# Kernel optimization log

Measured on AMD Instinct MI355X. Metric: run time of the kernel, lower is better.

The kernel has to match this reference:

```python
import jax, jax.numpy as jnp
import numpy as np

B, T, D, H, O = 64, 512, 512, 512, 1

def setup_inputs() -> dict:
    key = jax.random.key(0)
    ks = jax.random.split(key, 12)
    s_in = 1.0 / np.sqrt(H)
    inp = {
        'x': jax.random.normal(ks[0], (B, T, D), dtype=jnp.float32),
        'W_ih0': jax.random.uniform(ks[1], (H, D), jnp.float32, -s_in, s_in),
        'W_hh0': jax.random.uniform(ks[2], (H, H), jnp.float32, -s_in, s_in),
        'b_ih0': jax.random.uniform(ks[3], (H,), jnp.float32, -s_in, s_in),
        'b_hh0': jax.random.uniform(ks[4], (H,), jnp.float32, -s_in, s_in),
        'W_ih1': jax.random.uniform(ks[5], (H, H), jnp.float32, -s_in, s_in),
        'W_hh1': jax.random.uniform(ks[6], (H, H), jnp.float32, -s_in, s_in),
        'b_ih1': jax.random.uniform(ks[7], (H,), jnp.float32, -s_in, s_in),
        'b_hh1': jax.random.uniform(ks[8], (H,), jnp.float32, -s_in, s_in),
        'W_fc': jax.random.uniform(ks[9], (O, H), jnp.float32, -s_in, s_in),
        'b_fc': jax.random.uniform(ks[10], (O,), jnp.float32, -s_in, s_in),
    }
    return inp

def _rnn_layer(inp, W_ih, W_hh, b_ih, b_hh):
    # inp: [B, T, Din] -> [B, T, H].  h_t = tanh(x_t W_ih^T + b_ih + h_{t-1} W_hh^T + b_hh)
    xproj = jnp.einsum('btd,hd->bth', inp, W_ih) + b_ih + b_hh  # precompute input projection
    h0 = jnp.zeros((inp.shape[0], W_hh.shape[0]), inp.dtype)
    def step(h, xp):  # xp: [B, H]
        h = jnp.tanh(xp + h @ W_hh.T)
        return h, h
    _, outs = jax.lax.scan(step, h0, jnp.swapaxes(xproj, 0, 1))  # [T, B, H]
    return jnp.swapaxes(outs, 0, 1)

def reference(x, W_ih0, W_hh0, b_ih0, b_hh0, W_ih1, W_hh1, b_ih1, b_hh1, W_fc, b_fc):
    h = _rnn_layer(x, W_ih0, W_hh0, b_ih0, b_hh0)
    h = _rnn_layer(h, W_ih1, W_hh1, b_ih1, b_hh1)
    last = h[:, -1, :]                      # [B, H]
    return last @ W_fc.T + b_fc             # [B, O]
```

## Files before the change

kernel.cpp:

```cpp
#include <hip/hip_runtime.h>
#include <cstdint>
#include <cstddef>

typedef _Float16 f16;
typedef _Float16 half2_t __attribute__((ext_vector_type(2)));
typedef _Float16 half4_t __attribute__((ext_vector_type(4)));
typedef _Float16 half8_t __attribute__((ext_vector_type(8)));
typedef float floatx4 __attribute__((ext_vector_type(4)));

__device__ __forceinline__ float fdot2u(uint32_t w, uint32_t h, float acc) {
#if __has_builtin(__builtin_amdgcn_fdot2)
    return __builtin_amdgcn_fdot2(__builtin_bit_cast(half2_t, w),
                                  __builtin_bit_cast(half2_t, h), acc, false);
#else
    half2_t a = __builtin_bit_cast(half2_t, w);
    half2_t b = __builtin_bit_cast(half2_t, h);
    return acc + (float)a[0] * (float)b[0] + (float)a[1] * (float)b[1];
#endif
}

__device__ __forceinline__ void spin_ge(int* f, int v) {
    while (__hip_atomic_load(f, __ATOMIC_RELAXED, __HIP_MEMORY_SCOPE_AGENT) < v)
        __builtin_amdgcn_s_sleep(16);
}

__device__ __forceinline__ void acq_fence() {
    __builtin_amdgcn_fence(__ATOMIC_ACQUIRE, "agent");
}

__global__ void cvt_kernel(const float* __restrict__ in, f16* __restrict__ out, int n4) {
    int i = blockIdx.x * blockDim.x + threadIdx.x;
    int stride = gridDim.x * blockDim.x;
    const float4* in4 = (const float4*)in;
    for (; i < n4; i += stride) {
        float4 v = in4[i];
        half4_t h = {(f16)v.x, (f16)v.y, (f16)v.z, (f16)v.w};
        *(half4_t*)&out[(size_t)i * 4] = h;
    }
}

__global__ void bsum_kernel(const float* __restrict__ a, const float* __restrict__ b,
                            float* __restrict__ o) {
    int i = threadIdx.x;
    o[i] = a[i] + b[i];
}

__global__ void pack_whh(const float* __restrict__ W, uint32_t* __restrict__ wp) {
    int id = blockIdx.x * 256 + threadIdx.x;
    int j = id >> 8;
    int kp = id & 255;
    int k = kp * 2;
    int w = j >> 6, jsub = (j >> 3) & 7, r = j & 7;
    int kg = k >> 6, c = (k >> 3) & 7, q = (k >> 1) & 3;
    int tid = w * 64 + jsub * 8 + kg;
    int idx = c * 32 + r * 4 + q;
    uint32_t lo = (uint32_t)__builtin_bit_cast(uint16_t, (f16)W[(size_t)j * 512 + k]);
    uint32_t hi = (uint32_t)__builtin_bit_cast(uint16_t, (f16)W[(size_t)j * 512 + k + 1]);
    size_t off;
    if (idx < 224) off = (size_t)idx * 512 + tid;
    else           off = (size_t)224 * 512 + ((size_t)(r * 512 + tid)) * 4 + q;
    wp[off] = (hi << 16) | lo;
}

__global__ __launch_bounds__(256) void gemm_xp(const f16* __restrict__ A,
                                               const f16* __restrict__ Bw,
                                               const float* __restrict__ bias,
                                               f16* __restrict__ C) {
    const int bn = blockIdx.x & 3;
    const int bm = blockIdx.x >> 2;
    const int tid = threadIdx.x;
    const int w = tid >> 6, l = tid & 63;
    const int wr = w >> 1, wc = w & 1;
    __shared__ f16 As[128 * 32];
    __shared__ f16 Bs[128 * 32];
    floatx4 acc[4][4] = {};
    const int lr = l & 15, lk = (l >> 4) * 8;
    for (int kk = 0; kk < 512; kk += 32) {
        __syncthreads();
        uint4 av[2], bv[2];
#pragma unroll
        for (int s = 0; s < 2; ++s) {
            int chunk = tid + s * 256;
            int row = chunk >> 2;
            int colh = (chunk & 3) * 8;
            av[s] = *(const uint4*)&A[((size_t)(bm * 128 + row)) * 512 + kk + colh];
            bv[s] = *(const uint4*)&Bw[((size_t)(bn * 128 + row)) * 512 + kk + colh];
        }
#pragma unroll
        for (int s = 0; s < 2; ++s) {
            int chunk = tid + s * 256;
            *(uint4*)&As[chunk * 8] = av[s];
            *(uint4*)&Bs[chunk * 8] = bv[s];
        }
        __syncthreads();
        half8_t af[4], bf[4];
#pragma unroll
        for (int m = 0; m < 4; ++m)
            af[m] = *(const half8_t*)&As[(wr * 64 + m * 16 + lr) * 32 + lk];
#pragma unroll
        for (int n = 0; n < 4; ++n)
            bf[n] = *(const half8_t*)&Bs[(wc * 64 + n * 16 + lr) * 32 + lk];
#pragma unroll
        for (int m = 0; m < 4; ++m)
#pragma unroll
            for (int n = 0; n < 4; ++n)
                acc[m][n] = __builtin_amdgcn_mfma_f32_16x16x32_f16(af[m], bf[n], acc[m][n], 0, 0, 0);
    }
    float bz[4];
#pragma unroll
    for (int n = 0; n < 4; ++n) bz[n] = bias[bn * 128 + wc * 64 + n * 16 + lr];
    const int lq = l >> 4;
#pragma unroll
    for (int m = 0; m < 4; ++m)
#pragma unroll
        for (int n = 0; n < 4; ++n)
#pragma unroll
            for (int e = 0; e < 4; ++e) {
                int row = bm * 128 + wr * 64 + m * 16 + lq * 4 + e;
                int col = bn * 128 + wc * 64 + n * 16 + lr;
                C[(size_t)row * 512 + col] = (f16)(acc[m][n][e] + bz[n]);
            }
}

#define FOR_Q(M, c, r) M(c, r, 0) M(c, r, 1) M(c, r, 2) M(c, r, 3)
#define FOR_R8(M, c) FOR_Q(M, c, 0) FOR_Q(M, c, 1) FOR_Q(M, c, 2) FOR_Q(M, c, 3) \
                     FOR_Q(M, c, 4) FOR_Q(M, c, 5) FOR_Q(M, c, 6) FOR_Q(M, c, 7)
#define FOR_ALL(M) FOR_R8(M, 0) FOR_R8(M, 1) FOR_R8(M, 2) FOR_R8(M, 3) \
                   FOR_R8(M, 4) FOR_R8(M, 5) FOR_R8(M, 6)

#define DECLW(c, r, q) uint32_t W_##c##_##r##_##q;
#define LOADW(c, r, q) W_##c##_##r##_##q = wpb[(size_t)(((c)*32 + (r)*4 + (q)) * 512) + tid];
#define DOTQ(c, r, q) a##r = fdot2u(W_##c##_##r##_##q, hq##q, a##r);

#define CHUNK(c)                                                   \
    {                                                              \
        uint4 hv = *(const uint4*)(hrow + (c) * 4);                \
        uint32_t hq0 = hv.x, hq1 = hv.y, hq2 = hv.z, hq3 = hv.w;   \
        FOR_R8(DOTQ, c)                                            \
    }

#define LROW(r)                                                    \
    {                                                              \
        uint4 wv = *(const uint4*)&wlds[((r) * 512 + tid) * 4];    \
        a##r = fdot2u(wv.x, hq0, a##r);                            \
        a##r = fdot2u(wv.y, hq1, a##r);                            \
        a##r = fdot2u(wv.z, hq2, a##r);                            \
        a##r = fdot2u(wv.w, hq3, a##r);                            \
    }

#define CHUNKL                                                     \
    {                                                              \
        uint4 hv = *(const uint4*)(hrow + 7 * 4);                  \
        uint32_t hq0 = hv.x, hq1 = hv.y, hq2 = hv.z, hq3 = hv.w;   \
        LROW(0) LROW(1) LROW(2) LROW(3)                            \
        LROW(4) LROW(5) LROW(6) LROW(7)                            \
    }

#define TREE8                                                                 \
    float b0 = (m0 ? a1 : a0) + __shfl_xor(m0 ? a0 : a1, 1);                  \
    float b1 = (m0 ? a3 : a2) + __shfl_xor(m0 ? a2 : a3, 1);                  \
    float b2 = (m0 ? a5 : a4) + __shfl_xor(m0 ? a4 : a5, 1);                  \
    float b3 = (m0 ? a7 : a6) + __shfl_xor(m0 ? a6 : a7, 1);                  \
    float c0 = (m1 ? b1 : b0) + __shfl_xor(m1 ? b0 : b1, 2);                  \
    float c1 = (m1 ? b3 : b2) + __shfl_xor(m1 ? b2 : b3, 2);                  \
    float d0 = (m2 ? c1 : c0) + __shfl_xor(m2 ? c0 : c1, 4);

#define HB_STRIDE 72
#define XROW 576

__global__ __launch_bounds__(512)
__attribute__((amdgpu_waves_per_eu(2, 2)))
void fused3(const f16* __restrict__ xp0, const uint32_t* __restrict__ wp0,
            const uint32_t* __restrict__ wpih1, const uint32_t* __restrict__ wp1,
            const float* __restrict__ bs1,
            f16* __restrict__ h0seq, f16* __restrict__ xp1seq,
            f16* __restrict__ h1last,
            int* __restrict__ flag1, int* __restrict__ flag2) {
    const int xcd = blockIdx.x & 7;
    if (xcd >= 6) return;
    const int stage = xcd >> 1;
    const int row = (xcd & 1) * 32 + (blockIdx.x >> 3);
    const int tid = threadIdx.x;
    const int kg = tid & 7;
    __shared__ alignas(16) f16 hbuf[2][8 * HB_STRIDE];
    __shared__ uint32_t wlds[8 * 512 * 4];
    __shared__ alignas(16) f16 xin[2][16 * XROW];

    const uint32_t* wpb = (stage == 0) ? wp0 : (stage == 1) ? wpih1 : wp1;
    const f16* inbase = (stage == 0) ? xp0 + (size_t)row * 262144
                       : (stage == 1) ? h0seq + (size_t)row * 262144
                                      : xp1seq + (size_t)row * 262144;
    f16* outbase = (stage == 0) ? h0seq + (size_t)row * 262144
                  : (stage == 1) ? xp1seq + (size_t)row * 262144
                                 : h1last + (size_t)row * 512;
    int* flIn  = (stage == 1) ? flag1 + row : (stage == 2) ? flag2 + row : nullptr;
    int* flOut = (stage == 0) ? flag1 + row : (stage == 1) ? flag2 + row : nullptr;

    auto stageChunk = [&](int g) {
#pragma unroll
        for (int s2 = 0; s2 < 2; ++s2) {
            int s = tid + s2 * 512;
            int rw = s >> 6, pos = s & 63;
            uint4 v = *(const uint4*)&inbase[(size_t)(g * 16 + rw) * 512 + pos * 8];
            *(uint4*)&xin[g & 1][rw * XROW + (pos >> 3) * 72 + (pos & 7) * 8] = v;
        }
    };

    FOR_ALL(DECLW)
    FOR_ALL(LOADW)
#pragma unroll
    for (int i = 0; i < 8; ++i) {
        uint4 v = *(const uint4*)&wpb[(size_t)224 * 512 + (size_t)(i * 512 + tid) * 4];
        *(uint4*)&wlds[(i * 512 + tid) * 4] = v;
    }
    for (int i = tid; i < 2 * 8 * HB_STRIDE; i += 512) ((f16*)hbuf)[i] = (f16)0.f;
    float bsv = (stage == 1) ? bs1[tid] : 0.f;

    if (flIn) {
        spin_ge(flIn, 1);
        acq_fence();
    }
    stageChunk(0);
    __syncthreads();

    const bool m0 = (tid & 1), m1 = (tid & 2), m2 = (tid & 4);
    const int hwpos = (tid >> 6) * HB_STRIDE + (tid & 63);

    if (stage == 1) {
        for (int c = 0; c < 32; ++c) {
            for (int lt = 0; lt < 16; ++lt) {
                if (lt == 12 && c < 31) {
                    spin_ge(flIn, c + 2);
                    acq_fence();
                    stageChunk(c + 1);
                }
                float a0 = 0.f, a1 = 0.f, a2 = 0.f, a3 = 0.f;
                float a4 = 0.f, a5 = 0.f, a6 = 0.f, a7 = 0.f;
                const uint32_t* hrow = (const uint32_t*)&xin[c & 1][lt * XROW + kg * 72];
                CHUNKL
                CHUNK(0) CHUNK(1) CHUNK(2) CHUNK(3) CHUNK(4) CHUNK(5) CHUNK(6)
                TREE8
                outbase[(size_t)(c * 16 + lt) * 512 + tid] = (f16)(d0 + bsv);
            }
            __syncthreads();
            if (tid == 0)
                __hip_atomic_store(flOut, c + 1, __ATOMIC_RELEASE, __HIP_MEMORY_SCOPE_AGENT);
        }
    } else {
        int p = 0;
        for (int t = 0; t < 512; ++t) {
            const int c = t >> 4, lt = t & 15;
            if (lt == 12 && c < 31) {
                if (flIn) {
                    spin_ge(flIn, c + 2);
                    acq_fence();
                }
                stageChunk(c + 1);
            }
            float xpv = (float)xin[c & 1][lt * XROW + (tid >> 6) * 72 + (tid & 63)];

            float a0 = 0.f, a1 = 0.f, a2 = 0.f, a3 = 0.f;
            float a4 = 0.f, a5 = 0.f, a6 = 0.f, a7 = 0.f;
            const uint32_t* hrow = (const uint32_t*)&hbuf[p][kg * HB_STRIDE];
            CHUNKL
            CHUNK(0) CHUNK(1) CHUNK(2) CHUNK(3) CHUNK(4) CHUNK(5) CHUNK(6)
            TREE8
            float s = d0 + xpv;
            float e = __expf(2.0f * s);
            f16 hh = (f16)(1.0f - 2.0f / (1.0f + e));
            hbuf[p ^ 1][hwpos] = hh;
            if (stage == 0) outbase[(size_t)t * 512 + tid] = hh;
            else if (t == 511) outbase[tid] = hh;
            __syncthreads();
            if (stage == 0 && lt == 15 && tid == 0)
                __hip_atomic_store(flOut, c + 1, __ATOMIC_RELEASE, __HIP_MEMORY_SCOPE_AGENT);
            p ^= 1;
        }
    }
}

__global__ __launch_bounds__(512) void fc_kernel(const f16* __restrict__ h1,
                                                 const float* __restrict__ Wfc,
                                                 const float* __restrict__ bfc,
                                                 float* __restrict__ out) {
    int b = blockIdx.x, tid = threadIdx.x;
    __shared__ float red[8];
    float v = (float)h1[(size_t)b * 512 + tid] * Wfc[tid];
#pragma unroll
    for (int off = 32; off > 0; off >>= 1) v += __shfl_down(v, off, 64);
    if ((tid & 63) == 0) red[tid >> 6] = v;
    __syncthreads();
    if (tid == 0) {
        float s = bfc[0];
#pragma unroll
        for (int g = 0; g < 8; ++g) s += red[g];
        out[b] = s;
    }
}

extern "C" void kernel_launch(void* const* d_in, const int* in_sizes, int n_in,
                              void* d_out, int out_size, void* d_ws, size_t ws_size,
                              hipStream_t stream) {
    const float* x    = (const float*)d_in[0];
    const float* Wih0 = (const float*)d_in[1];
    const float* Whh0 = (const float*)d_in[2];
    const float* bih0 = (const float*)d_in[3];
    const float* bhh0 = (const float*)d_in[4];
    const float* Wih1 = (const float*)d_in[5];
    const float* Whh1 = (const float*)d_in[6];
    const float* bih1 = (const float*)d_in[7];
    const float* bhh1 = (const float*)d_in[8];
    const float* Wfc  = (const float*)d_in[9];
    const float* bfc  = (const float*)d_in[10];
    float* out = (float*)d_out;

    char* ws = (char*)d_ws;
    size_t off = 0;
    auto alloc = [&](size_t bytes) -> void* {
        void* p = ws + off;
        off += (bytes + 255) & ~(size_t)255;
        return p;
    };
    const size_t MTD = (size_t)64 * 512 * 512;
    f16* x16    = (f16*)alloc(MTD * 2);
    f16* h016   = (f16*)alloc(MTD * 2);
    f16* xpb    = (f16*)alloc(MTD * 2);
    f16* xp1b   = (f16*)alloc(MTD * 2);
    f16* wih016 = (f16*)alloc((size_t)512 * 512 * 2);
    uint32_t* wp0   = (uint32_t*)alloc((size_t)131072 * 4);
    uint32_t* wp1   = (uint32_t*)alloc((size_t)131072 * 4);
    uint32_t* wpih1 = (uint32_t*)alloc((size_t)131072 * 4);
    float* bs0 = (float*)alloc(512 * 4);
    float* bs1 = (float*)alloc(512 * 4);
    f16* h1last = (f16*)alloc((size_t)64 * 512 * 2);
    int* flags = (int*)alloc(128 * 4);

    cvt_kernel<<<2048, 256, 0, stream>>>(x, x16, (int)(MTD / 4));
    cvt_kernel<<<256, 256, 0, stream>>>(Wih0, wih016, 512 * 512 / 4);
    bsum_kernel<<<1, 512, 0, stream>>>(bih0, bhh0, bs0);
    bsum_kernel<<<1, 512, 0, stream>>>(bih1, bhh1, bs1);
    pack_whh<<<512, 256, 0, stream>>>(Whh0, wp0);
    pack_whh<<<512, 256, 0, stream>>>(Whh1, wp1);
    pack_whh<<<512, 256, 0, stream>>>(Wih1, wpih1);
    (void)hipMemsetAsync(flags, 0, 128 * 4, stream);

    gemm_xp<<<1024, 256, 0, stream>>>(x16, wih016, bs0, xpb);
    fused3<<<256, 512, 0, stream>>>(xpb, wp0, wpih1, wp1, bs1,
                                    h016, xp1b, h1last, flags, flags + 64);
    fc_kernel<<<64, 512, 0, stream>>>(h1last, Wfc, bfc, out);
}
```

Baseline: 1.172 ms.

## Halve inter-stage chunk size and prefetch up to three chunks ahead

Measured after the change: 1.489 ms. 27.1% more time.

```diff
diff --git a/kernel.cpp b/kernel.cpp
--- a/kernel.cpp
+++ b/kernel.cpp
@@ -184,7 +184,8 @@
     const int kg = tid & 7;
     __shared__ alignas(16) f16 hbuf[2][8 * HB_STRIDE];
     __shared__ uint32_t wlds[8 * 512 * 4];
-    __shared__ alignas(16) f16 xin[2][16 * XROW];
+    __shared__ alignas(16) f16 xin[4][8 * XROW];
+    __shared__ int availLds;
 
     const uint32_t* wpb = (stage == 0) ? wp0 : (stage == 1) ? wpih1 : wp1;
     const f16* inbase = (stage == 0) ? xp0 + (size_t)row * 262144
@@ -197,13 +198,9 @@
     int* flOut = (stage == 0) ? flag1 + row : (stage == 1) ? flag2 + row : nullptr;
 
     auto stageChunk = [&](int g) {
-#pragma unroll
-        for (int s2 = 0; s2 < 2; ++s2) {
-            int s = tid + s2 * 512;
-            int rw = s >> 6, pos = s & 63;
-            uint4 v = *(const uint4*)&inbase[(size_t)(g * 16 + rw) * 512 + pos * 8];
-            *(uint4*)&xin[g & 1][rw * XROW + (pos >> 3) * 72 + (pos & 7) * 8] = v;
-        }
+        int rw = tid >> 6, pos = tid & 63;
+        uint4 v = *(const uint4*)&inbase[(size_t)(g * 8 + rw) * 512 + pos * 8];
+        *(uint4*)&xin[g & 3][rw * XROW + (pos >> 3) * 72 + (pos & 7) * 8] = v;
     };
 
     FOR_ALL(DECLW)
@@ -227,37 +224,65 @@
     const int hwpos = (tid >> 6) * HB_STRIDE + (tid & 63);
 
     if (stage == 1) {
-        for (int c = 0; c < 32; ++c) {
-            for (int lt = 0; lt < 16; ++lt) {
-                if (lt == 12 && c < 31) {
-                    spin_ge(flIn, c + 2);
-                    acq_fence();
-                    stageChunk(c + 1);
+        int fetched = 0, availB = 1;
+        for (int c = 0; c < 64; ++c) {
+            for (int lt = 0; lt < 8; ++lt) {
+                if (lt == 4) {
+                    if (fetched < c + 1 && c < 63) {
+                        spin_ge(flIn, c + 2);
+                        acq_fence();
+                        stageChunk(c + 1);
+                        fetched = c + 1;
+                    }
+                    int lim = (c + 3 < 63) ? c + 3 : 63;
+                    int target = (availB - 1 < lim) ? availB - 1 : lim;
+                    if (target > fetched) {
+                        acq_fence();
+                        for (int g = fetched + 1; g <= target; ++g) stageChunk(g);
+                        fetched = target;
+                    }
                 }
                 float a0 = 0.f, a1 = 0.f, a2 = 0.f, a3 = 0.f;
                 float a4 = 0.f, a5 = 0.f, a6 = 0.f, a7 = 0.f;
-                const uint32_t* hrow = (const uint32_t*)&xin[c & 1][lt * XROW + kg * 72];
+                const uint32_t* hrow = (const uint32_t*)&xin[c & 3][lt * XROW + kg * 72];
                 CHUNKL
                 CHUNK(0) CHUNK(1) CHUNK(2) CHUNK(3) CHUNK(4) CHUNK(5) CHUNK(6)
                 TREE8
-                outbase[(size_t)(c * 16 + lt) * 512 + tid] = (f16)(d0 + bsv);
+                outbase[(size_t)(c * 8 + lt) * 512 + tid] = (f16)(d0 + bsv);
             }
+            if (tid == 0)
+                availLds = __hip_atomic_load(flIn, __ATOMIC_RELAXED, __HIP_MEMORY_SCOPE_AGENT);
             __syncthreads();
+            availB = availLds;
             if (tid == 0)
                 __hip_atomic_store(flOut, c + 1, __ATOMIC_RELEASE, __HIP_MEMORY_SCOPE_AGENT);
         }
     } else {
-        int p = 0;
+        int p = 0, fetched = 0;
         for (int t = 0; t < 512; ++t) {
-            const int c = t >> 4, lt = t & 15;
-            if (lt == 12 && c < 31) {
-                if (flIn) {
-                    spin_ge(flIn, c + 2);
-                    acq_fence();
+            const int c = t >> 3, lt = t & 7;
+            if (flIn) {
+                if (lt == 3 && tid == 0)
+                    availLds = __hip_atomic_load(flIn, __ATOMIC_RELAXED, __HIP_MEMORY_SCOPE_AGENT);
+                if (lt == 4) {
+                    if (fetched < c + 1 && c < 63) {
+                        spin_ge(flIn, c + 2);
+                        acq_fence();
+                        stageChunk(c + 1);
+                        fetched = c + 1;
+                    }
+                    int lim = (c + 3 < 63) ? c + 3 : 63;
+                    int target = (availLds - 1 < lim) ? availLds - 1 : lim;
+                    if (target > fetched) {
+                        acq_fence();
+                        for (int g = fetched + 1; g <= target; ++g) stageChunk(g);
+                        fetched = target;
+                    }
                 }
-                stageChunk(c + 1);
+            } else {
+                if (lt == 4 && c < 63) stageChunk(c + 1);
             }
-            float xpv = (float)xin[c & 1][lt * XROW + (tid >> 6) * 72 + (tid & 63)];
+            float xpv = (float)xin[c & 3][lt * XROW + (tid >> 6) * 72 + (tid & 63)];
 
             float a0 = 0.f, a1 = 0.f, a2 = 0.f, a3 = 0.f;
             float a4 = 0.f, a5 = 0.f, a6 = 0.f, a7 = 0.f;
@@ -272,7 +297,7 @@
             if (stage == 0) outbase[(size_t)t * 512 + tid] = hh;
             else if (t == 511) outbase[tid] = hh;
             __syncthreads();
-            if (stage == 0 && lt == 15 && tid == 0)
+            if (stage == 0 && lt == 7 && tid == 0)
                 __hip_atomic_store(flOut, c + 1, __ATOMIC_RELEASE, __HIP_MEMORY_SCOPE_AGENT);
             p ^= 1;
         }
```
